# Kernel optimization log

Measured on AMD Instinct MI355X. Metric: run time of the kernel, lower is better.

Reference implementation:

```python
import jax, jax.numpy as jnp
import numpy as np

N = 8192
IN_CH = 256
OUT_CH = 256


def setup_inputs() -> dict:
    key = jax.random.key(0)
    k1, k2, k3, k4, k5 = jax.random.split(key, 5)
    features = jax.random.normal(k1, (N, IN_CH), dtype=jnp.float32)
    wavelets = jax.random.normal(k2, (N, N), dtype=jnp.float32)
    wavelets_inv = jax.random.normal(k3, (N, N), dtype=jnp.float32)
    # parameters
    # xavier uniform for weight_matrix
    limit = np.sqrt(6.0 / (IN_CH + OUT_CH)).astype(np.float32)
    weight_matrix = jax.random.uniform(k4, (IN_CH, OUT_CH), minval=-limit, maxval=limit, dtype=jnp.float32)
    filt = jax.random.uniform(k5, (N,), minval=0.9, maxval=1.1, dtype=jnp.float32)
    return {"features": features, "wavelets": wavelets, "wavelets_inv": wavelets_inv,
            "weight_matrix": weight_matrix, "filt": filt}


def reference(features, wavelets, wavelets_inv, weight_matrix, filt):
    # transformed = features @ W                    [N, out]
    transformed = features @ weight_matrix
    # spectral = wavelets_inv @ transformed         [N, out]
    spectral = wavelets_inv @ transformed
    # torch.diag(filter) @ spectral == filt[:, None] * spectral (avoid NxN diag GEMM)
    filtered = filt[:, None] * spectral
    # output = wavelets @ filtered                  [N, out]
    return wavelets @ filtered
```

## Files before the change

### kernel.cpp

```cpp
#include <hip/hip_runtime.h>
#include <hip/hip_bf16.h>
#include <stdint.h>
#include <stddef.h>

typedef __bf16 bf16;
typedef float f32x4 __attribute__((ext_vector_type(4)));
typedef bf16 bf16x8 __attribute__((ext_vector_type(8)));
typedef bf16 bf16x4 __attribute__((ext_vector_type(4)));

#define MROWS 8192
#define NOUT 256
#define BM 32
#define BK 128
#define NTHREADS 512

#define LDS_A_BYTES (BM * BK * 2)

#define SCHED0 __builtin_amdgcn_sched_barrier(0)
#define SBAR __builtin_amdgcn_s_barrier()


template <bool SCALE, bool OUTT>
__global__ __launch_bounds__(NTHREADS, 1) void gemm_fused(
    const float* __restrict__ A, const bf16* __restrict__ Bp,
    const float* __restrict__ filt, void* __restrict__ outp,
    const int K, const int lda) {
  __shared__ char lds[2][LDS_A_BYTES];
  const int t = threadIdx.x;
  const int w = t >> 6;
  const int l = t & 63;
  const int m0 = blockIdx.x * BM;
  const int NT = K / BK;

  const int ar = t >> 4;
  const int acb = t & 15;
  const float* gA = A + (size_t)(m0 + ar) * (size_t)lda + acb * 8;
  const int a_lds_off = (ar * (BK * 2) + acb * 16) ^ ((ar & 7) << 4);

  int aoff[2][4];
#pragma unroll
  for (int af = 0; af < 2; ++af)
#pragma unroll
    for (int ak = 0; ak < 4; ++ak) {
      const int r = af * 16 + (l & 15);
      const int kb = ak * 64 + (l >> 4) * 16;
      aoff[af][ak] = (r * (BK * 2) + kb) ^ ((r & 7) << 4);
    }

  const char* pBw = (const char*)Bp + w * 8192 + l * 16;

  f32x4 acc[2][2] = {};

  f32x4 aS0a = __builtin_nontemporal_load((const f32x4*)gA);
  f32x4 aS0b = __builtin_nontemporal_load((const f32x4*)gA + 1);
  f32x4 aS1a = __builtin_nontemporal_load((const f32x4*)(gA + BK));
  f32x4 aS1b = __builtin_nontemporal_load((const f32x4*)(gA + BK) + 1);
  bf16x8 Bc[2][4], Bn[2][4];
#pragma unroll
  for (int bfi = 0; bfi < 2; ++bfi)
#pragma unroll
    for (int ak = 0; ak < 4; ++ak)
      Bc[bfi][ak] = *(const bf16x8*)(pBw + (bfi * 4 + ak) * 1024);
  {
    bf16x8 pk;
#pragma unroll
    for (int j = 0; j < 4; ++j) {
      pk[j] = (bf16)aS0a[j];
      pk[j + 4] = (bf16)aS0b[j];
    }
    *(bf16x8*)(lds[0] + a_lds_off) = pk;
  }
  asm volatile("s_waitcnt lgkmcnt(0)" ::: "memory");
  SBAR;
  SCHED0;

#define BODY(TS, P, BCUR, BNXT, AW0, AW1, AL0, AL1)                           \
  {                                                                           \
    const char* bb = lds[P];                                                  \
    bf16x8 afr[2][4];                                                         \
    _Pragma("unroll") for (int af = 0; af < 2; ++af)                          \
        _Pragma("unroll") for (int ak = 0; ak < 4; ++ak)                      \
            afr[af][ak] = *(const bf16x8*)(bb + aoff[af][ak]);                \
    SCHED0;                                                                   \
    const size_t kb1 = (size_t)((((TS) + 1) < NT ? ((TS) + 1) : 0)) << 16;    \
    _Pragma("unroll") for (int bfi = 0; bfi < 2; ++bfi)                       \
        _Pragma("unroll") for (int ak = 0; ak < 4; ++ak)                      \
            BNXT[bfi][ak] =                                                   \
                *(const bf16x8*)(pBw + kb1 + (bfi * 4 + ak) * 1024);          \
    SCHED0;                                                                   \
    const int ka2 = (((TS) + 2) < NT ? ((TS) + 2) : 0) * BK;                  \
    AL0 = __builtin_nontemporal_load((const f32x4*)(gA + ka2));               \
    AL1 = __builtin_nontemporal_load((const f32x4*)(gA + ka2) + 1);           \
    SCHED0;                                                                   \
    asm volatile("s_waitcnt lgkmcnt(0)" ::: "memory");                        \
    SCHED0;                                                                   \
    __builtin_amdgcn_s_setprio(1);                                            \
    _Pragma("unroll") for (int ak = 0; ak < 4; ++ak)                          \
        _Pragma("unroll") for (int af = 0; af < 2; ++af)                      \
            _Pragma("unroll") for (int bfi = 0; bfi < 2; ++bfi)               \
                acc[af][bfi] = __builtin_amdgcn_mfma_f32_16x16x32_bf16(       \
                    afr[af][ak], BCUR[bfi][ak], acc[af][bfi], 0, 0, 0);       \
    __builtin_amdgcn_s_setprio(0);                                            \
    SCHED0;                                                                   \
    {                                                                         \
      bf16x8 pk;                                                              \
      _Pragma("unroll") for (int j = 0; j < 4; ++j) {                         \
        pk[j] = (bf16)AW0[j];                                                 \
        pk[j + 4] = (bf16)AW1[j];                                             \
      }                                                                       \
      *(bf16x8*)(lds[P ^ 1] + a_lds_off) = pk;                                \
    }                                                                         \
    asm volatile("s_waitcnt lgkmcnt(0)" ::: "memory");                        \
    SBAR;                                                                     \
    SCHED0;                                                                   \
  }

  for (int ts = 0; ts < NT; ts += 2) {
    BODY(ts, 0, Bc, Bn, aS1a, aS1b, aS0a, aS0b);
    BODY(ts + 1, 1, Bn, Bc, aS0a, aS0b, aS1a, aS1b);
  }
#undef BODY

#pragma unroll
  for (int af = 0; af < 2; ++af)
#pragma unroll
    for (int bfi = 0; bfi < 2; ++bfi) {
      const int mb = m0 + af * 16 + (l >> 4) * 4;
      const int n = w * 32 + bfi * 16 + (l & 15);
      f32x4 v = acc[af][bfi];
      if (SCALE) {
#pragma unroll
        for (int j = 0; j < 4; ++j) v[j] *= filt[mb + j];
      }
      if (OUTT) {
        bf16x4 pv;
#pragma unroll
        for (int j = 0; j < 4; ++j) pv[j] = (bf16)v[j];
        const int ts = mb >> 7, wq = n >> 5, bq = (n >> 4) & 1, aq = (mb >> 5) & 3;
        const int lq = ((mb >> 3) & 3) * 16 + (n & 15);
        char* dst = (char*)outp +
                    (size_t)(((ts * 64 + wq * 8 + bq * 4 + aq) << 10) + lq * 16 +
                             (mb & 7) * 2);
        *(bf16x4*)dst = pv;
      } else {
        float* po = (float*)outp + (size_t)mb * NOUT + n;
#pragma unroll
        for (int j = 0; j < 4; ++j) po[(size_t)j * NOUT] = v[j];
      }
    }
}

__global__ void prep_wt(const float* __restrict__ W, bf16* __restrict__ Wp) {
  const int k = blockIdx.x;
  const int n = threadIdx.x;
  const int off = (((k >> 7) * 64 + (n >> 5) * 8 + ((n >> 4) & 1) * 4 +
                    ((k >> 5) & 3)) << 10) +
                  (((k >> 3) & 3) * 16 + (n & 15)) * 16 + (k & 7) * 2;
  *(bf16*)((char*)Wp + off) = (bf16)W[k * 256 + n];
}

extern "C" void kernel_launch(void* const* d_in, const int* in_sizes, int n_in,
                              void* d_out, int out_size, void* d_ws, size_t ws_size,
                              hipStream_t stream) {
  const float* features = (const float*)d_in[0];
  const float* wavelets = (const float*)d_in[1];
  const float* wavelets_inv = (const float*)d_in[2];
  const float* W = (const float*)d_in[3];
  const float* filt = (const float*)d_in[4];
  float* out = (float*)d_out;

  char* ws = (char*)d_ws;
  bf16* Wp = (bf16*)ws;
  bf16* Tp = (bf16*)(ws + 131072);
  bf16* Fp = (bf16*)(ws + 131072 + 4194304);

  prep_wt<<<256, 256, 0, stream>>>(W, Wp);
  gemm_fused<false, true><<<256, NTHREADS, 0, stream>>>(features, Wp, nullptr, Tp, 256, 256);
  gemm_fused<true, true><<<256, NTHREADS, 0, stream>>>(wavelets_inv, Tp, filt, Fp, 8192, 8192);
  gemm_fused<false, false><<<256, NTHREADS, 0, stream>>>(wavelets, Fp, nullptr, out, 8192, 8192);
}
```

Before: 192.1 us.

## Deepen software pipeline for large GEMMs with 4-stage LDS ring and fragment prefetch

Adds a gemm_deep kernel for the two 8192-K GEMMs that uses a 4-buffer LDS ring. Global A loads are issued three tiles ahead, and the A fragments for the next tile are read from LDS into registers before the current MFMA block runs. The aim is to hide HBM latency and LDS read latency behind the MFMAs in these memory-bound streaming GEMMs. In exchange it uses more LDS and registers (two fragment sets plus two B sets), and it assumes NT is a multiple of 4.

```diff
diff --git a/kernel.cpp b/kernel.cpp
--- a/kernel.cpp
+++ b/kernel.cpp
@@ -21,7 +21,146 @@
 
 
 template <bool SCALE, bool OUTT>
-__global__ __launch_bounds__(NTHREADS, 1) void gemm_fused(
+__global__ __launch_bounds__(NTHREADS, 1) void gemm_deep(
+    const float* __restrict__ A, const bf16* __restrict__ Bp,
+    const float* __restrict__ filt, void* __restrict__ outp,
+    const int K, const int lda) {
+  __shared__ char lds[4][LDS_A_BYTES];
+  const int t = threadIdx.x;
+  const int w = t >> 6;
+  const int l = t & 63;
+  const int m0 = blockIdx.x * BM;
+  const int NT = K / BK;
+
+  const int ar = t >> 4;
+  const int acb = t & 15;
+  const float* gA = A + (size_t)(m0 + ar) * (size_t)lda + acb * 8;
+  const int a_lds_off = (ar * (BK * 2) + acb * 16) ^ ((ar & 7) << 4);
+
+  int aoff[2][4];
+#pragma unroll
+  for (int af = 0; af < 2; ++af)
+#pragma unroll
+    for (int ak = 0; ak < 4; ++ak) {
+      const int r = af * 16 + (l & 15);
+      const int kb = ak * 64 + (l >> 4) * 16;
+      aoff[af][ak] = (r * (BK * 2) + kb) ^ ((r & 7) << 4);
+    }
+
+  const char* pBw = (const char*)Bp + w * 8192 + l * 16;
+
+  f32x4 acc[2][2] = {};
+
+  f32x4 A0a = __builtin_nontemporal_load((const f32x4*)gA);
+  f32x4 A0b = __builtin_nontemporal_load((const f32x4*)gA + 1);
+  f32x4 A1a = __builtin_nontemporal_load((const f32x4*)(gA + BK));
+  f32x4 A1b = __builtin_nontemporal_load((const f32x4*)(gA + BK) + 1);
+  bf16x8 B0[2][4], B1[2][4];
+#pragma unroll
+  for (int bfi = 0; bfi < 2; ++bfi)
+#pragma unroll
+    for (int ak = 0; ak < 4; ++ak)
+      B0[bfi][ak] = *(const bf16x8*)(pBw + (bfi * 4 + ak) * 1024);
+  f32x4 g0a = __builtin_nontemporal_load((const f32x4*)(gA + 2 * BK));
+  f32x4 g0b = __builtin_nontemporal_load((const f32x4*)(gA + 2 * BK) + 1);
+  f32x4 g1a, g1b;
+  {
+    bf16x8 pk;
+#pragma unroll
+    for (int j = 0; j < 4; ++j) { pk[j] = (bf16)A0a[j]; pk[j + 4] = (bf16)A0b[j]; }
+    *(bf16x8*)(lds[0] + a_lds_off) = pk;
+#pragma unroll
+    for (int j = 0; j < 4; ++j) { pk[j] = (bf16)A1a[j]; pk[j + 4] = (bf16)A1b[j]; }
+    *(bf16x8*)(lds[1] + a_lds_off) = pk;
+  }
+  asm volatile("s_waitcnt lgkmcnt(0)" ::: "memory");
+  SBAR;
+  SCHED0;
+  bf16x8 f0[2][4], f1[2][4];
+#pragma unroll
+  for (int af = 0; af < 2; ++af)
+#pragma unroll
+    for (int ak = 0; ak < 4; ++ak)
+      f0[af][ak] = *(const bf16x8*)(lds[0] + aoff[af][ak]);
+  SCHED0;
+
+#define BODY_D(TS, SW, SR, FC, FN, BCr, BNr, AC0, AC1, AN0, AN1)              \
+  {                                                                           \
+    const size_t kb1 = (size_t)((((TS) + 1) < NT ? ((TS) + 1) : 0)) << 16;    \
+    _Pragma("unroll") for (int bfi = 0; bfi < 2; ++bfi)                       \
+        _Pragma("unroll") for (int ak = 0; ak < 4; ++ak)                      \
+            BNr[bfi][ak] =                                                    \
+                *(const bf16x8*)(pBw + kb1 + (bfi * 4 + ak) * 1024);          \
+    SCHED0;                                                                   \
+    const int ka3 = ((((TS) + 3) < NT) ? ((TS) + 3) : 0) * BK;                \
+    AN0 = __builtin_nontemporal_load((const f32x4*)(gA + ka3));               \
+    AN1 = __builtin_nontemporal_load((const f32x4*)(gA + ka3) + 1);           \
+    SCHED0;                                                                   \
+    {                                                                         \
+      bf16x8 pk;                                                              \
+      _Pragma("unroll") for (int j = 0; j < 4; ++j) {                         \
+        pk[j] = (bf16)AC0[j];                                                 \
+        pk[j + 4] = (bf16)AC1[j];                                             \
+      }                                                                       \
+      *(bf16x8*)(lds[SW] + a_lds_off) = pk;                                   \
+    }                                                                         \
+    SCHED0;                                                                   \
+    _Pragma("unroll") for (int af = 0; af < 2; ++af)                          \
+        _Pragma("unroll") for (int ak = 0; ak < 4; ++ak)                      \
+            FN[af][ak] = *(const bf16x8*)(lds[SR] + aoff[af][ak]);            \
+    SCHED0;                                                                   \
+    __builtin_amdgcn_s_setprio(1);                                            \
+    _Pragma("unroll") for (int ak = 0; ak < 4; ++ak)                          \
+        _Pragma("unroll") for (int af = 0; af < 2; ++af)                      \
+            _Pragma("unroll") for (int bfi = 0; bfi < 2; ++bfi)               \
+                acc[af][bfi] = __builtin_amdgcn_mfma_f32_16x16x32_bf16(       \
+                    FC[af][ak], BCr[bfi][ak], acc[af][bfi], 0, 0, 0);         \
+    __builtin_amdgcn_s_setprio(0);                                            \
+    SCHED0;                                                                   \
+    asm volatile("s_waitcnt lgkmcnt(0)" ::: "memory");                        \
+    SBAR;                                                                     \
+    SCHED0;                                                                   \
+  }
+
+  for (int ts = 0; ts < NT; ts += 4) {
+    BODY_D(ts, 2, 1, f0, f1, B0, B1, g0a, g0b, g1a, g1b);
+    BODY_D(ts + 1, 3, 2, f1, f0, B1, B0, g1a, g1b, g0a, g0b);
+    BODY_D(ts + 2, 0, 3, f0, f1, B0, B1, g0a, g0b, g1a, g1b);
+    BODY_D(ts + 3, 1, 0, f1, f0, B1, B0, g1a, g1b, g0a, g0b);
+  }
+#undef BODY_D
+
+#pragma unroll
+  for (int af = 0; af < 2; ++af)
+#pragma unroll
+    for (int bfi = 0; bfi < 2; ++bfi) {
+      const int mb = m0 + af * 16 + (l >> 4) * 4;
+      const int n = w * 32 + bfi * 16 + (l & 15);
+      f32x4 v = acc[af][bfi];
+      if (SCALE) {
+#pragma unroll
+        for (int j = 0; j < 4; ++j) v[j] *= filt[mb + j];
+      }
+      if (OUTT) {
+        bf16x4 pv;
+#pragma unroll
+        for (int j = 0; j < 4; ++j) pv[j] = (bf16)v[j];
+        const int tsq = mb >> 7, wq = n >> 5, bq = (n >> 4) & 1, aq = (mb >> 5) & 3;
+        const int lq = ((mb >> 3) & 3) * 16 + (n & 15);
+        char* dst = (char*)outp +
+                    (size_t)(((tsq * 64 + wq * 8 + bq * 4 + aq) << 10) + lq * 16 +
+                             (mb & 7) * 2);
+        *(bf16x4*)dst = pv;
+      } else {
+        float* po = (float*)outp + (size_t)mb * NOUT + n;
+#pragma unroll
+        for (int j = 0; j < 4; ++j) po[(size_t)j * NOUT] = v[j];
+      }
+    }
+}
+
+template <bool SCALE, bool OUTT>
+__global__ __launch_bounds__(NTHREADS, 1) void gemm_small(
     const float* __restrict__ A, const bf16* __restrict__ Bp,
     const float* __restrict__ filt, void* __restrict__ outp,
     const int K, const int lda) {
@@ -64,17 +203,14 @@
   {
     bf16x8 pk;
 #pragma unroll
-    for (int j = 0; j < 4; ++j) {
-      pk[j] = (bf16)aS0a[j];
-      pk[j + 4] = (bf16)aS0b[j];
-    }
+    for (int j = 0; j < 4; ++j) { pk[j] = (bf16)aS0a[j]; pk[j + 4] = (bf16)aS0b[j]; }
     *(bf16x8*)(lds[0] + a_lds_off) = pk;
   }
   asm volatile("s_waitcnt lgkmcnt(0)" ::: "memory");
   SBAR;
   SCHED0;
 
-#define BODY(TS, P, BCUR, BNXT, AW0, AW1, AL0, AL1)                           \
+#define BODY_S(TS, P, BCUR, BNXT, AW0, AW1, AL0, AL1)                         \
   {                                                                           \
     const char* bb = lds[P];                                                  \
     bf16x8 afr[2][4];                                                         \
@@ -116,10 +252,10 @@
   }
 
   for (int ts = 0; ts < NT; ts += 2) {
-    BODY(ts, 0, Bc, Bn, aS1a, aS1b, aS0a, aS0b);
-    BODY(ts + 1, 1, Bn, Bc, aS0a, aS0b, aS1a, aS1b);
-  }
-#undef BODY
+    BODY_S(ts, 0, Bc, Bn, aS1a, aS1b, aS0a, aS0b);
+    BODY_S(ts + 1, 1, Bn, Bc, aS0a, aS0b, aS1a, aS1b);
+  }
+#undef BODY_S
 
 #pragma unroll
   for (int af = 0; af < 2; ++af)
@@ -136,10 +272,10 @@
         bf16x4 pv;
 #pragma unroll
         for (int j = 0; j < 4; ++j) pv[j] = (bf16)v[j];
-        const int ts = mb >> 7, wq = n >> 5, bq = (n >> 4) & 1, aq = (mb >> 5) & 3;
+        const int tsq = mb >> 7, wq = n >> 5, bq = (n >> 4) & 1, aq = (mb >> 5) & 3;
         const int lq = ((mb >> 3) & 3) * 16 + (n & 15);
         char* dst = (char*)outp +
-                    (size_t)(((ts * 64 + wq * 8 + bq * 4 + aq) << 10) + lq * 16 +
+                    (size_t)(((tsq * 64 + wq * 8 + bq * 4 + aq) << 10) + lq * 16 +
                              (mb & 7) * 2);
         *(bf16x4*)dst = pv;
       } else {
@@ -175,7 +311,7 @@
   bf16* Fp = (bf16*)(ws + 131072 + 4194304);
 
   prep_wt<<<256, 256, 0, stream>>>(W, Wp);
-  gemm_fused<false, true><<<256, NTHREADS, 0, stream>>>(features, Wp, nullptr, Tp, 256, 256);
-  gemm_fused<true, true><<<256, NTHREADS, 0, stream>>>(wavelets_inv, Tp, filt, Fp, 8192, 8192);
-  gemm_fused<false, false><<<256, NTHREADS, 0, stream>>>(wavelets, Fp, nullptr, out, 8192, 8192);
+  gemm_small<false, true><<<256, NTHREADS, 0, stream>>>(features, Wp, nullptr, Tp, 256, 256);
+  gemm_deep<true, true><<<256, NTHREADS, 0, stream>>>(wavelets_inv, Tp, filt, Fp, 8192, 8192);
+  gemm_deep<false, false><<<256, NTHREADS, 0, stream>>>(wavelets, Fp, nullptr, out, 8192, 8192);
 }
```

After: 194.3 us. Within noise of the previous version (+1.1%).
